# Kernel optimization log

Measured on AMD Instinct MI355X. Metric: run time of the kernel, lower is better.

Reference implementation:

```python
import jax, jax.numpy as jnp
import numpy as np

N, A, C = 4096, 512, 100


def setup_inputs() -> dict:
    key = jax.random.key(0)
    k1, k2, k3 = jax.random.split(key, 3)
    features = jax.random.normal(k1, (N, A), dtype=jnp.float32)
    y_s = jax.random.normal(k2, (N, C), dtype=jnp.float32)
    labels = jax.random.randint(k3, (N,), 0, C, dtype=jnp.int64)
    CoVariance = jnp.zeros((C, A, A), dtype=jnp.float32)
    Ave = jnp.zeros((C, A), dtype=jnp.float32)
    Amount = jnp.zeros((C,), dtype=jnp.float32)
    return {"features": features, "y_s": y_s, "CoVariance": CoVariance,
            "Ave": Ave, "Amount": Amount, "labels": labels}


def reference(features, y_s, CoVariance, Ave, Amount, labels):
    n, a = features.shape
    c = Ave.shape[0]
    dt = features.dtype

    onehot = jax.nn.one_hot(labels, c, dtype=dt)            # [N, C]
    counts = onehot.sum(axis=0)                             # [C]
    counts_safe = jnp.where(counts == 0, 1.0, counts)       # Amount_CxA==0 -> 1

    # per-class mean: ave_CxA [C, A]
    sum_feats = onehot.T @ features                          # [C, A]
    ave_CxA = sum_feats / counts_safe[:, None]

    # centered features w.r.t. own-class mean; masked per-class copies
    centered = features - ave_CxA[labels]                    # [N, A]
    masked = onehot.T[:, :, None] * centered[None, :, :]     # [C, N, A]
    # per-class scatter of outer products (equals torch bmm over zero-padded rows)
    var_temp = jnp.einsum('cna,nb->cab', masked, centered) / counts_safe[:, None, None]

    # mixing weights; NaN (0/0) -> 0
    denom = counts + Amount                                  # [C]
    w = jnp.where(denom > 0, counts / denom, 0.0)            # [C]

    ave_old = jax.lax.stop_gradient(Ave)                     # .detach() in torch
    cov_old = jax.lax.stop_gradient(CoVariance)
    diff = ave_old - ave_CxA                                 # [C, A]
    additional_CV = (w * (1.0 - w))[:, None, None] * jnp.einsum('ca,cb->cab', diff, diff)

    new_cov = cov_old * (1.0 - w)[:, None, None] + var_temp * w[:, None, None] + additional_CV
    new_ave = ave_old * (1.0 - w)[:, None] + ave_CxA * w[:, None]
    new_amount = Amount + counts

    logp = jax.nn.log_softmax(y_s, axis=-1)                  # [N, C]
    loss = -jnp.mean(jnp.take_along_axis(logp, labels[:, None], axis=1))

    return loss, new_cov, new_ave, new_amount
```

## Files before the change

kernel.cpp:

```cpp
#include <hip/hip_runtime.h>


#define TM 128
#define KC 16
#define LSTR 132
#define LZ 16

typedef float nf4 __attribute__((ext_vector_type(4)));

__global__ __launch_bounds__(1024) void prep_kernel(
    const int* __restrict__ labels, const float* __restrict__ Amount,
    int* __restrict__ offsets, int* __restrict__ idx_sorted,
    float* __restrict__ w_arr, float* __restrict__ inv_cs,
    float* __restrict__ amount_out, float* __restrict__ out_loss0, int N, int C) {
    __shared__ int hist[1024];
    __shared__ int offs[1025];
    __shared__ int cur[1024];
    const int tid = threadIdx.x;
    for (int c = tid; c < C; c += 1024) { hist[c] = 0; cur[c] = 0; }
    __syncthreads();
    for (int i = tid; i < N; i += 1024) atomicAdd(&hist[labels[i]], 1);
    __syncthreads();
    if (tid == 0) {
        int o = 0;
        for (int c = 0; c < C; ++c) { offs[c] = o; o += hist[c]; }
        offs[C] = o;
    }
    __syncthreads();
    for (int c = tid; c < C; c += 1024) {
        float cf = (float)hist[c];
        float cs = cf > 0.f ? cf : 1.f;
        inv_cs[c] = 1.f / cs;
        float am = Amount[c];
        float dn = cf + am;
        w_arr[c] = dn > 0.f ? cf / dn : 0.f;
        amount_out[c] = am + cf;
        offsets[c] = offs[c];
    }
    if (tid == 0) { offsets[C] = offs[C]; out_loss0[0] = 0.f; }
    for (int i = tid; i < N; i += 1024) {
        int c = labels[i];
        int p = atomicAdd(&cur[c], 1);
        idx_sorted[offs[c] + p] = i;
    }
}

__global__ __launch_bounds__(512) void ave_kernel(
    const float* __restrict__ feats, const float* __restrict__ Ave_in,
    const int* __restrict__ idx_sorted, const int* __restrict__ offsets,
    const float* __restrict__ w_arr, const float* __restrict__ inv_cs,
    float* __restrict__ ave_new, float* __restrict__ ave_out, int A) {
    __shared__ int idxs[512];
    const int c = blockIdx.x;
    const int base = offsets[c];
    const int nc = offsets[c + 1] - base;
    const float w = w_arr[c];
    const float ic = inv_cs[c];
    for (int col = threadIdx.x; col < A; col += blockDim.x) {
        float sum = 0.f;
        for (int i0 = 0; i0 < nc; i0 += 512) {
            int chunk = min(512, nc - i0);
            __syncthreads();
            for (int j = threadIdx.x; j < chunk; j += blockDim.x)
                idxs[j] = idx_sorted[base + i0 + j];
            __syncthreads();
            int j = 0;
            for (; j + 3 < chunk; j += 4) {
                float f0 = feats[(size_t)idxs[j] * A + col];
                float f1 = feats[(size_t)idxs[j + 1] * A + col];
                float f2 = feats[(size_t)idxs[j + 2] * A + col];
                float f3 = feats[(size_t)idxs[j + 3] * A + col];
                sum += f0 + f1 + f2 + f3;
            }
            for (; j < chunk; ++j) sum += feats[(size_t)idxs[j] * A + col];
        }
        float av = sum * ic;
        ave_new[(size_t)c * A + col] = av;
        ave_out[(size_t)c * A + col] = Ave_in[(size_t)c * A + col] * (1.f - w) + av * w;
    }
}

__global__ __launch_bounds__(256) void cov_kernel(
    const float* __restrict__ feats, const float* __restrict__ cov_in,
    const float* __restrict__ ave_new, const float* __restrict__ Ave_in,
    const float* __restrict__ y_s, const int* __restrict__ labels,
    const int* __restrict__ idx_sorted, const int* __restrict__ offsets,
    const float* __restrict__ w_arr, const float* __restrict__ inv_cs,
    float* __restrict__ out_cov, float* __restrict__ out_loss0,
    int N, int C, int A, float invN) {

    if ((int)blockIdx.z >= C) {
        __shared__ float bsum[4];
        const int lane = threadIdx.x & 63;
        const int wv = threadIdx.x >> 6;
        const int bxy = blockIdx.y * gridDim.x + blockIdx.x;
        const int bid = (blockIdx.z - C) * (gridDim.x * gridDim.y) + bxy;
        const int nwaves = LZ * gridDim.x * gridDim.y * 4;
        const int gw = bid * 4 + wv;
        float wsum = 0.f;
        for (int r = gw; r < N; r += nwaves) {
            const float* row = y_s + (size_t)r * C;
            float m = -1e30f;
            for (int col = lane; col < C; col += 64) m = fmaxf(m, row[col]);
            #pragma unroll
            for (int off = 32; off > 0; off >>= 1) m = fmaxf(m, __shfl_xor(m, off));
            float se = 0.f;
            for (int col = lane; col < C; col += 64) se += __expf(row[col] - m);
            #pragma unroll
            for (int off = 32; off > 0; off >>= 1) se += __shfl_xor(se, off);
            if (lane == 0) wsum += -(row[labels[r]] - m - __logf(se));
        }
        if (lane == 0) bsum[wv] = wsum;
        __syncthreads();
        if (threadIdx.x == 0)
            atomicAdd(out_loss0, (bsum[0] + bsum[1] + bsum[2] + bsum[3]) * invN);
        return;
    }

    const int c  = blockIdx.z;
    const int a0 = blockIdx.y * TM;
    const int b0 = blockIdx.x * TM;
    const int tid = threadIdx.x;

    __shared__ float Xa[KC][LSTR];
    __shared__ float Xb[KC][LSTR];
    __shared__ float aveA[TM], aveB[TM], dA[TM], dB[TM];

    if (tid < TM) {
        float av = ave_new[(size_t)c * A + a0 + tid];
        aveA[tid] = av;
        dA[tid] = Ave_in[(size_t)c * A + a0 + tid] - av;
    } else {
        int t = tid - TM;
        float bv = ave_new[(size_t)c * A + b0 + t];
        aveB[t] = bv;
        dB[t] = Ave_in[(size_t)c * A + b0 + t] - bv;
    }

    const float w   = w_arr[c];
    const float omw = 1.f - w;
    const float s   = inv_cs[c] * w;
    const float aw  = w * omw;
    const size_t cbase = (size_t)c * A * A;
    const int ty = tid >> 4, tx = tid & 15;

    if (s > 0.f) {
        const int base = offsets[c];
        const int nc = offsets[c + 1] - base;
        const int li = ty;
        const int cg = tx * 4;
        const int nchunks = (nc + KC - 1) / KC;

        __syncthreads();

        float4 v0, v1, v2, v3;
        {
            v0 = make_float4(0.f, 0.f, 0.f, 0.f); v1 = v0; v2 = v0; v3 = v0;
            if (li < nc) {
                int row = idx_sorted[base + li];
                const float* fr = feats + (size_t)row * A;
                v0 = *reinterpret_cast<const float4*>(fr + a0 + cg);
                v1 = *reinterpret_cast<const float4*>(fr + a0 + cg + 64);
                v2 = *reinterpret_cast<const float4*>(fr + b0 + cg);
                v3 = *reinterpret_cast<const float4*>(fr + b0 + cg + 64);
                v0.x -= aveA[cg];      v0.y -= aveA[cg + 1];  v0.z -= aveA[cg + 2];  v0.w -= aveA[cg + 3];
                v1.x -= aveA[cg + 64]; v1.y -= aveA[cg + 65]; v1.z -= aveA[cg + 66]; v1.w -= aveA[cg + 67];
                v2.x -= aveB[cg];      v2.y -= aveB[cg + 1];  v2.z -= aveB[cg + 2];  v2.w -= aveB[cg + 3];
                v3.x -= aveB[cg + 64]; v3.y -= aveB[cg + 65]; v3.z -= aveB[cg + 66]; v3.w -= aveB[cg + 67];
            }
        }

        float acc[2][4][2][4] = {};
        if (omw != 0.f) {
            const float sc = omw / s;
            #pragma unroll
            for (int ri = 0; ri < 2; ++ri)
                #pragma unroll
                for (int i = 0; i < 4; ++i) {
                    const size_t rowo = cbase + (size_t)(a0 + ri * 64 + ty * 4 + i) * A + b0;
                    #pragma unroll
                    for (int ci = 0; ci < 2; ++ci) {
                        float4 co = *reinterpret_cast<const float4*>(&cov_in[rowo + ci * 64 + tx * 4]);
                        acc[ri][i][ci][0] = co.x * sc;
                        acc[ri][i][ci][1] = co.y * sc;
                        acc[ri][i][ci][2] = co.z * sc;
                        acc[ri][i][ci][3] = co.w * sc;
                    }
                }
        }

        for (int ch = 0; ch < nchunks; ++ch) {
            __syncthreads();
            *reinterpret_cast<float4*>(&Xa[li][cg])      = v0;
            *reinterpret_cast<float4*>(&Xa[li][cg + 64]) = v1;
            *reinterpret_cast<float4*>(&Xb[li][cg])      = v2;
            *reinterpret_cast<float4*>(&Xb[li][cg + 64]) = v3;
            __syncthreads();

            if (ch + 1 < nchunks) {
                const int kk = (ch + 1) * KC;
                v0 = make_float4(0.f, 0.f, 0.f, 0.f); v1 = v0; v2 = v0; v3 = v0;
                if (kk + li < nc) {
                    int row = idx_sorted[base + kk + li];
                    const float* fr = feats + (size_t)row * A;
                    v0 = *reinterpret_cast<const float4*>(fr + a0 + cg);
                    v1 = *reinterpret_cast<const float4*>(fr + a0 + cg + 64);
                    v2 = *reinterpret_cast<const float4*>(fr + b0 + cg);
                    v3 = *reinterpret_cast<const float4*>(fr + b0 + cg + 64);
                    v0.x -= aveA[cg];      v0.y -= aveA[cg + 1];  v0.z -= aveA[cg + 2];  v0.w -= aveA[cg + 3];
                    v1.x -= aveA[cg + 64]; v1.y -= aveA[cg + 65]; v1.z -= aveA[cg + 66]; v1.w -= aveA[cg + 67];
                    v2.x -= aveB[cg];      v2.y -= aveB[cg + 1];  v2.z -= aveB[cg + 2];  v2.w -= aveB[cg + 3];
                    v3.x -= aveB[cg + 64]; v3.y -= aveB[cg + 65]; v3.z -= aveB[cg + 66]; v3.w -= aveB[cg + 67];
                }
            }

            const int kn = min(KC, nc - ch * KC);
            if (kn == KC) {
                #pragma unroll
                for (int k = 0; k < KC; ++k) {
                    float4 a0v = *reinterpret_cast<const float4*>(&Xa[k][ty * 4]);
                    float4 a1v = *reinterpret_cast<const float4*>(&Xa[k][64 + ty * 4]);
                    float4 b0v = *reinterpret_cast<const float4*>(&Xb[k][tx * 4]);
                    float4 b1v = *reinterpret_cast<const float4*>(&Xb[k][64 + tx * 4]);
                    float af[2][4] = {{a0v.x, a0v.y, a0v.z, a0v.w}, {a1v.x, a1v.y, a1v.z, a1v.w}};
                    float bf[2][4] = {{b0v.x, b0v.y, b0v.z, b0v.w}, {b1v.x, b1v.y, b1v.z, b1v.w}};
                    #pragma unroll
                    for (int ri = 0; ri < 2; ++ri)
                        #pragma unroll
                        for (int i = 0; i < 4; ++i)
                            #pragma unroll
                            for (int ci = 0; ci < 2; ++ci)
                                #pragma unroll
                                for (int j = 0; j < 4; ++j)
                                    acc[ri][i][ci][j] += af[ri][i] * bf[ci][j];
                }
            } else {
                for (int k = 0; k < kn; ++k) {
                    float4 a0v = *reinterpret_cast<const float4*>(&Xa[k][ty * 4]);
                    float4 a1v = *reinterpret_cast<const float4*>(&Xa[k][64 + ty * 4]);
                    float4 b0v = *reinterpret_cast<const float4*>(&Xb[k][tx * 4]);
                    float4 b1v = *reinterpret_cast<const float4*>(&Xb[k][64 + tx * 4]);
                    float af[2][4] = {{a0v.x, a0v.y, a0v.z, a0v.w}, {a1v.x, a1v.y, a1v.z, a1v.w}};
                    float bf[2][4] = {{b0v.x, b0v.y, b0v.z, b0v.w}, {b1v.x, b1v.y, b1v.z, b1v.w}};
                    #pragma unroll
                    for (int ri = 0; ri < 2; ++ri)
                        #pragma unroll
                        for (int i = 0; i < 4; ++i)
                            #pragma unroll
                            for (int ci = 0; ci < 2; ++ci)
                                #pragma unroll
                                for (int j = 0; j < 4; ++j)
                                    acc[ri][i][ci][j] += af[ri][i] * bf[ci][j];
                }
            }
        }

        float db[2][4];
        #pragma unroll
        for (int ci = 0; ci < 2; ++ci)
            #pragma unroll
            for (int j = 0; j < 4; ++j) db[ci][j] = dB[ci * 64 + tx * 4 + j];

        #pragma unroll
        for (int ri = 0; ri < 2; ++ri)
            #pragma unroll
            for (int i = 0; i < 4; ++i) {
                float da = aw * dA[ri * 64 + ty * 4 + i];
                const size_t rowo = cbase + (size_t)(a0 + ri * 64 + ty * 4 + i) * A + b0;
                #pragma unroll
                for (int ci = 0; ci < 2; ++ci) {
                    nf4 res;
                    res.x = acc[ri][i][ci][0] * s + da * db[ci][0];
                    res.y = acc[ri][i][ci][1] * s + da * db[ci][1];
                    res.z = acc[ri][i][ci][2] * s + da * db[ci][2];
                    res.w = acc[ri][i][ci][3] * s + da * db[ci][3];
                    __builtin_nontemporal_store(res,
                        reinterpret_cast<nf4*>(&out_cov[rowo + ci * 64 + tx * 4]));
                }
            }
    } else {
        for (int t = tid; t < TM * TM / 4; t += 256) {
            const int r = t >> 5;
            const int c4 = (t & 31) * 4;
            const size_t o = cbase + (size_t)(a0 + r) * A + b0 + c4;
            float4 co = *reinterpret_cast<const float4*>(&cov_in[o]);
            nf4 res;
            res.x = co.x * omw; res.y = co.y * omw; res.z = co.z * omw; res.w = co.w * omw;
            __builtin_nontemporal_store(res, reinterpret_cast<nf4*>(&out_cov[o]));
        }
    }
}

extern "C" void kernel_launch(void* const* d_in, const int* in_sizes, int n_in,
                              void* d_out, int out_size, void* d_ws, size_t ws_size,
                              hipStream_t stream) {
    const float* feats  = (const float*)d_in[0];
    const float* y_s    = (const float*)d_in[1];
    const float* cov_in = (const float*)d_in[2];
    const float* Ave_in = (const float*)d_in[3];
    const float* Amount = (const float*)d_in[4];
    const int*   labels = (const int*)d_in[5];

    const int C = in_sizes[4];
    const int N = in_sizes[5];
    const int A = in_sizes[3] / C;

    float* out      = (float*)d_out;
    float* out_loss = out;
    float* out_cov  = out + 1;
    float* out_ave  = out_cov + (size_t)C * A * A;
    float* out_amt  = out_ave + (size_t)C * A;

    char* w8 = (char*)d_ws;
    int* offsets    = (int*)w8;   w8 += (size_t)(C + 1) * sizeof(int);
    int* idx_sorted = (int*)w8;   w8 += (size_t)N * sizeof(int);
    float* w_arr    = (float*)w8; w8 += (size_t)C * sizeof(float);
    float* inv_cs   = (float*)w8; w8 += (size_t)C * sizeof(float);
    float* ave_new  = (float*)w8; w8 += (size_t)C * A * sizeof(float);

    prep_kernel<<<1, 1024, 0, stream>>>(labels, Amount, offsets, idx_sorted,
                                        w_arr, inv_cs, out_amt, out_loss, N, C);
    ave_kernel<<<C, 512, 0, stream>>>(feats, Ave_in, idx_sorted, offsets,
                                      w_arr, inv_cs, ave_new, out_ave, A);
    dim3 grid(A / TM, A / TM, C + LZ);
    cov_kernel<<<grid, 256, 0, stream>>>(feats, cov_in, ave_new, Ave_in, y_s, labels,
                                         idx_sorted, offsets, w_arr, inv_cs,
                                         out_cov, out_loss, N, C, A, 1.f / (float)N);
}
```

Baseline: 224.3 us.

## Drop separate mean kernel; compute uncentered scatter and subtract mean outer product

The separate ave_kernel launch goes away. Each cov tile now accumulates the raw feature scatter plus per-column sums, derives the class mean locally, and applies the identity sum(x-mu)(x-mu)^T = sum xx^T - n*mu*mu^T when writing out. The new average output is produced by extra blocks appended to the same cov launch. This removes a kernel launch and the dependency on a precomputed mean, at the cost of possible precision loss from the uncentered formula plus extra reductions and syncs per tile.

New measurement: 241.2 us. 7.5% more time.

```diff
diff --git a/kernel.cpp b/kernel.cpp
--- a/kernel.cpp
+++ b/kernel.cpp
@@ -45,49 +45,61 @@
     }
 }
 
-__global__ __launch_bounds__(512) void ave_kernel(
-    const float* __restrict__ feats, const float* __restrict__ Ave_in,
+__global__ __launch_bounds__(256) void cov_kernel(
+    const float* __restrict__ feats, const float* __restrict__ cov_in,
+    const float* __restrict__ Ave_in, const float* __restrict__ y_s,
+    const int* __restrict__ labels,
     const int* __restrict__ idx_sorted, const int* __restrict__ offsets,
     const float* __restrict__ w_arr, const float* __restrict__ inv_cs,
-    float* __restrict__ ave_new, float* __restrict__ ave_out, int A) {
-    __shared__ int idxs[512];
-    const int c = blockIdx.x;
-    const int base = offsets[c];
-    const int nc = offsets[c + 1] - base;
-    const float w = w_arr[c];
-    const float ic = inv_cs[c];
-    for (int col = threadIdx.x; col < A; col += blockDim.x) {
-        float sum = 0.f;
-        for (int i0 = 0; i0 < nc; i0 += 512) {
-            int chunk = min(512, nc - i0);
-            __syncthreads();
-            for (int j = threadIdx.x; j < chunk; j += blockDim.x)
-                idxs[j] = idx_sorted[base + i0 + j];
-            __syncthreads();
-            int j = 0;
-            for (; j + 3 < chunk; j += 4) {
-                float f0 = feats[(size_t)idxs[j] * A + col];
-                float f1 = feats[(size_t)idxs[j + 1] * A + col];
-                float f2 = feats[(size_t)idxs[j + 2] * A + col];
-                float f3 = feats[(size_t)idxs[j + 3] * A + col];
-                sum += f0 + f1 + f2 + f3;
-            }
-            for (; j < chunk; ++j) sum += feats[(size_t)idxs[j] * A + col];
-        }
-        float av = sum * ic;
-        ave_new[(size_t)c * A + col] = av;
-        ave_out[(size_t)c * A + col] = Ave_in[(size_t)c * A + col] * (1.f - w) + av * w;
-    }
-}
-
-__global__ __launch_bounds__(256) void cov_kernel(
-    const float* __restrict__ feats, const float* __restrict__ cov_in,
-    const float* __restrict__ ave_new, const float* __restrict__ Ave_in,
-    const float* __restrict__ y_s, const int* __restrict__ labels,
-    const int* __restrict__ idx_sorted, const int* __restrict__ offsets,
-    const float* __restrict__ w_arr, const float* __restrict__ inv_cs,
-    float* __restrict__ out_cov, float* __restrict__ out_loss0,
+    float* __restrict__ out_cov, float* __restrict__ out_ave,
+    float* __restrict__ out_loss0,
     int N, int C, int A, float invN) {
+
+    if ((int)blockIdx.z >= C + LZ) {
+        __shared__ int idxs[256];
+        const int nxy = gridDim.x * gridDim.y;
+        const int bid = ((int)blockIdx.z - C - LZ) * nxy
+                        + blockIdx.y * gridDim.x + blockIdx.x;
+        if (bid >= C) return;
+        const int c = bid;
+        const int tid = threadIdx.x;
+        const int base = offsets[c];
+        const int nc = offsets[c + 1] - base;
+        const float w = w_arr[c];
+        const float ic = inv_cs[c];
+        for (int c0 = 0; c0 < A; c0 += 512) {
+            const int colA = c0 + tid;
+            const int colB = c0 + 256 + tid;
+            float s0 = 0.f, s1 = 0.f;
+            for (int i0 = 0; i0 < nc; i0 += 256) {
+                int chunk = min(256, nc - i0);
+                __syncthreads();
+                if (tid < chunk) idxs[tid] = idx_sorted[base + i0 + tid];
+                __syncthreads();
+                int j = 0;
+                for (; j + 3 < chunk; j += 4) {
+                    const float* f0 = feats + (size_t)idxs[j] * A;
+                    const float* f1 = feats + (size_t)idxs[j + 1] * A;
+                    const float* f2 = feats + (size_t)idxs[j + 2] * A;
+                    const float* f3 = feats + (size_t)idxs[j + 3] * A;
+                    if (colA < A) s0 += f0[colA] + f1[colA] + f2[colA] + f3[colA];
+                    if (colB < A) s1 += f0[colB] + f1[colB] + f2[colB] + f3[colB];
+                }
+                for (; j < chunk; ++j) {
+                    const float* fr = feats + (size_t)idxs[j] * A;
+                    if (colA < A) s0 += fr[colA];
+                    if (colB < A) s1 += fr[colB];
+                }
+            }
+            if (colA < A)
+                out_ave[(size_t)c * A + colA] =
+                    Ave_in[(size_t)c * A + colA] * (1.f - w) + (s0 * ic) * w;
+            if (colB < A)
+                out_ave[(size_t)c * A + colB] =
+                    Ave_in[(size_t)c * A + colB] * (1.f - w) + (s1 * ic) * w;
+        }
+        return;
+    }
 
     if ((int)blockIdx.z >= C) {
         __shared__ float bsum[4];
@@ -124,18 +136,7 @@
 
     __shared__ float Xa[KC][LSTR];
     __shared__ float Xb[KC][LSTR];
-    __shared__ float aveA[TM], aveB[TM], dA[TM], dB[TM];
-
-    if (tid < TM) {
-        float av = ave_new[(size_t)c * A + a0 + tid];
-        aveA[tid] = av;
-        dA[tid] = Ave_in[(size_t)c * A + a0 + tid] - av;
-    } else {
-        int t = tid - TM;
-        float bv = ave_new[(size_t)c * A + b0 + t];
-        aveB[t] = bv;
-        dB[t] = Ave_in[(size_t)c * A + b0 + t] - bv;
-    }
+    __shared__ float muA[TM], muB[TM], dA[TM], dB[TM];
 
     const float w   = w_arr[c];
     const float omw = 1.f - w;
@@ -150,8 +151,6 @@
         const int li = ty;
         const int cg = tx * 4;
         const int nchunks = (nc + KC - 1) / KC;
-
-        __syncthreads();
 
         float4 v0, v1, v2, v3;
         {
@@ -163,12 +162,10 @@
                 v1 = *reinterpret_cast<const float4*>(fr + a0 + cg + 64);
                 v2 = *reinterpret_cast<const float4*>(fr + b0 + cg);
                 v3 = *reinterpret_cast<const float4*>(fr + b0 + cg + 64);
-                v0.x -= aveA[cg];      v0.y -= aveA[cg + 1];  v0.z -= aveA[cg + 2];  v0.w -= aveA[cg + 3];
-                v1.x -= aveA[cg + 64]; v1.y -= aveA[cg + 65]; v1.z -= aveA[cg + 66]; v1.w -= aveA[cg + 67];
-                v2.x -= aveB[cg];      v2.y -= aveB[cg + 1];  v2.z -= aveB[cg + 2];  v2.w -= aveB[cg + 3];
-                v3.x -= aveB[cg + 64]; v3.y -= aveB[cg + 65]; v3.z -= aveB[cg + 66]; v3.w -= aveB[cg + 67];
-            }
-        }
+            }
+        }
+
+        float4 sA0 = make_float4(0.f, 0.f, 0.f, 0.f), sA1 = sA0, sB0 = sA0, sB1 = sA0;
 
         float acc[2][4][2][4] = {};
         if (omw != 0.f) {
@@ -195,6 +192,10 @@
             *reinterpret_cast<float4*>(&Xa[li][cg + 64]) = v1;
             *reinterpret_cast<float4*>(&Xb[li][cg])      = v2;
             *reinterpret_cast<float4*>(&Xb[li][cg + 64]) = v3;
+            sA0.x += v0.x; sA0.y += v0.y; sA0.z += v0.z; sA0.w += v0.w;
+            sA1.x += v1.x; sA1.y += v1.y; sA1.z += v1.z; sA1.w += v1.w;
+            sB0.x += v2.x; sB0.y += v2.y; sB0.z += v2.z; sB0.w += v2.w;
+            sB1.x += v3.x; sB1.y += v3.y; sB1.z += v3.z; sB1.w += v3.w;
             __syncthreads();
 
             if (ch + 1 < nchunks) {
@@ -207,10 +208,6 @@
                     v1 = *reinterpret_cast<const float4*>(fr + a0 + cg + 64);
                     v2 = *reinterpret_cast<const float4*>(fr + b0 + cg);
                     v3 = *reinterpret_cast<const float4*>(fr + b0 + cg + 64);
-                    v0.x -= aveA[cg];      v0.y -= aveA[cg + 1];  v0.z -= aveA[cg + 2];  v0.w -= aveA[cg + 3];
-                    v1.x -= aveA[cg + 64]; v1.y -= aveA[cg + 65]; v1.z -= aveA[cg + 66]; v1.w -= aveA[cg + 67];
-                    v2.x -= aveB[cg];      v2.y -= aveB[cg + 1];  v2.z -= aveB[cg + 2];  v2.w -= aveB[cg + 3];
-                    v3.x -= aveB[cg + 64]; v3.y -= aveB[cg + 65]; v3.z -= aveB[cg + 66]; v3.w -= aveB[cg + 67];
                 }
             }
 
@@ -255,25 +252,54 @@
             }
         }
 
-        float db[2][4];
+        __syncthreads();
+        *reinterpret_cast<float4*>(&Xa[li][cg])      = sA0;
+        *reinterpret_cast<float4*>(&Xa[li][cg + 64]) = sA1;
+        *reinterpret_cast<float4*>(&Xb[li][cg])      = sB0;
+        *reinterpret_cast<float4*>(&Xb[li][cg + 64]) = sB1;
+        __syncthreads();
+        {
+            const int t = tid & 127;
+            float sum = 0.f;
+            if (tid < 128) {
+                #pragma unroll
+                for (int r = 0; r < KC; ++r) sum += Xa[r][t];
+                float mu = sum * inv_cs[c];
+                muA[t] = mu;
+                dA[t] = Ave_in[(size_t)c * A + a0 + t] - mu;
+            } else {
+                #pragma unroll
+                for (int r = 0; r < KC; ++r) sum += Xb[r][t];
+                float mu = sum * inv_cs[c];
+                muB[t] = mu;
+                dB[t] = Ave_in[(size_t)c * A + b0 + t] - mu;
+            }
+        }
+        __syncthreads();
+
+        float mb[2][4], db[2][4];
         #pragma unroll
         for (int ci = 0; ci < 2; ++ci)
             #pragma unroll
-            for (int j = 0; j < 4; ++j) db[ci][j] = dB[ci * 64 + tx * 4 + j];
+            for (int j = 0; j < 4; ++j) {
+                mb[ci][j] = muB[ci * 64 + tx * 4 + j];
+                db[ci][j] = dB[ci * 64 + tx * 4 + j];
+            }
 
         #pragma unroll
         for (int ri = 0; ri < 2; ++ri)
             #pragma unroll
             for (int i = 0; i < 4; ++i) {
+                float ma = w  * muA[ri * 64 + ty * 4 + i];
                 float da = aw * dA[ri * 64 + ty * 4 + i];
                 const size_t rowo = cbase + (size_t)(a0 + ri * 64 + ty * 4 + i) * A + b0;
                 #pragma unroll
                 for (int ci = 0; ci < 2; ++ci) {
                     nf4 res;
-                    res.x = acc[ri][i][ci][0] * s + da * db[ci][0];
-                    res.y = acc[ri][i][ci][1] * s + da * db[ci][1];
-                    res.z = acc[ri][i][ci][2] * s + da * db[ci][2];
-                    res.w = acc[ri][i][ci][3] * s + da * db[ci][3];
+                    res.x = acc[ri][i][ci][0] * s - ma * mb[ci][0] + da * db[ci][0];
+                    res.y = acc[ri][i][ci][1] * s - ma * mb[ci][1] + da * db[ci][1];
+                    res.z = acc[ri][i][ci][2] * s - ma * mb[ci][2] + da * db[ci][2];
+                    res.w = acc[ri][i][ci][3] * s - ma * mb[ci][3] + da * db[ci][3];
                     __builtin_nontemporal_store(res,
                         reinterpret_cast<nf4*>(&out_cov[rowo + ci * 64 + tx * 4]));
                 }
@@ -316,14 +342,15 @@
     int* idx_sorted = (int*)w8;   w8 += (size_t)N * sizeof(int);
     float* w_arr    = (float*)w8; w8 += (size_t)C * sizeof(float);
     float* inv_cs   = (float*)w8; w8 += (size_t)C * sizeof(float);
-    float* ave_new  = (float*)w8; w8 += (size_t)C * A * sizeof(float);
 
     prep_kernel<<<1, 1024, 0, stream>>>(labels, Amount, offsets, idx_sorted,
                                         w_arr, inv_cs, out_amt, out_loss, N, C);
-    ave_kernel<<<C, 512, 0, stream>>>(feats, Ave_in, idx_sorted, offsets,
-                                      w_arr, inv_cs, ave_new, out_ave, A);
-    dim3 grid(A / TM, A / TM, C + LZ);
-    cov_kernel<<<grid, 256, 0, stream>>>(feats, cov_in, ave_new, Ave_in, y_s, labels,
+
+    const int nxy = (A / TM) * (A / TM);
+    const int AZ = (C + nxy - 1) / nxy;
+    dim3 grid(A / TM, A / TM, C + LZ + AZ);
+    cov_kernel<<<grid, 256, 0, stream>>>(feats, cov_in, Ave_in, y_s, labels,
                                          idx_sorted, offsets, w_arr, inv_cs,
-                                         out_cov, out_loss, N, C, A, 1.f / (float)N);
+                                         out_cov, out_ave, out_loss, N, C, A,
+                                         1.f / (float)N);
 }
```
